# Kernel optimization log

Measured on AMD Instinct MI355X. Metric: run time of the kernel, lower is better.

The kernel has to match this reference:

```python
import jax, jax.numpy as jnp
import numpy as np

SIGMA_LOW = 0.2
SIGMA_HIGH = 0.01
DT = 0.1


def _gauss_kernel(sigma):
    # tw always uses sigma_low for its range, as in the original __init__
    tw = jnp.arange(-3.0 * SIGMA_LOW, 3.0 * SIGMA_LOW, 0.001 * DT, dtype=jnp.float32)  # 12000 taps
    g = jnp.exp(-0.5 * (tw / sigma) ** 2)
    return g / jnp.sum(g)


def _same_corr_fft(x, w):
    """tf.nn.conv1d(x, w_shared, stride=1, padding='SAME') where the same 1-D
    kernel w is applied to every channel independently (shared-weight depthwise).
    x: (1, T, C) NWC, w: (K,). FFT-based since K=12000 taps."""
    T = x.shape[1]
    K = w.shape[0]
    N = T + K - 1                      # full linear correlation length
    pad_left = (K - 1) // 2            # TF SAME left padding
    Xf = jnp.fft.rfft(x, n=N, axis=1)
    Wf = jnp.fft.rfft(w[::-1], n=N)    # flip kernel: correlation via convolution
    z = jnp.fft.irfft(Xf * Wf[None, :, None], n=N, axis=1)  # (1, N, C)
    start = K - 1 - pad_left           # offset of SAME output inside full result
    return jax.lax.dynamic_slice_in_dim(z, start, T, axis=1)


def setup_inputs() -> dict:
    key = jax.random.key(0)
    firings = jax.random.normal(key, (1, 100000, 512), dtype=jnp.float32)
    sel_idx = jnp.arange(256, dtype=jnp.int32)  # static boolean mask -> gather indices
    return {
        "firings": firings,
        "gauss_low": _gauss_kernel(SIGMA_LOW),
        "gauss_high": _gauss_kernel(SIGMA_HIGH),
        "sel_idx": sel_idx,
    }


def reference(firings, gauss_low, gauss_high, sel_idx):
    # boolean_mask(firings, mask, axis=2) -> channel gather
    sel = jnp.take(firings, sel_idx, axis=2)              # (1, T, Csel)
    low = _same_corr_fft(sel, gauss_low)                  # low-pass component
    filt = sel - low + jnp.mean(low)                      # high-pass + restore global mean
    return _same_corr_fft(filt, gauss_high)               # smooth with narrow Gaussian
```

## Files before the change

### kernel.cpp

```cpp
#include <hip/hip_runtime.h>
#include <hip/hip_bf16.h>

#define T_LEN   100000
#define C_SEL   256
#define C_IN    512
#define KLOW    12000
#define B1      50
#define NB1     2000
#define ND1     2001
#define NW1     241
#define ND2E    5003
#define WH_OFF  5500
#define KH      1001
#define MLEN    5000
#define TR      50
#define NBLK    2000
#define NAC     53
#define NSLOT   21
#define PROW    ((size_t)ND2E*C_SEL)

typedef __attribute__((ext_vector_type(4))) float f32x4;

__device__ __forceinline__ float rf(float x){
  return __int_as_float(__builtin_amdgcn_readfirstlane(__float_as_int(x)));
}

__device__ __forceinline__ void stage16(const float* g, float* l){
  __builtin_amdgcn_global_load_lds((const __attribute__((address_space(1))) void*)g,
                                   (__attribute__((address_space(3))) void*)l,
                                   16, 0, 0);
}

__global__ __launch_bounds__(256) void kA_prep(const float* __restrict__ wlow,
                                               const float* __restrict__ whigh,
                                               float* __restrict__ W1,
                                               float* __restrict__ musum,
                                               float* __restrict__ cwh,
                                               float* __restrict__ wht){
  if (blockIdx.x == 0){
    int m1 = threadIdx.x;
    if (m1 == 0) musum[0] = 0.f;
    if (m1 < NW1){
      float s = 0.f;
      int kbase = 50*m1 - 1;
      for (int off = 0; off < 50; ++off){
        int k = kbase + off;
        if (k >= 0 && k < KLOW) s += wlow[k];
      }
      W1[m1] = s * (1.0f/50.0f);
    }
    for (int k = threadIdx.x; k < 20*51; k += 256){
      int pp = k / 51, u = k - 51*pp;
      int j = 20*u + pp - 1;
      wht[k] = (j >= 0 && j < KH) ? whigh[WH_OFF + j] : 0.f;
    }
  } else {
    __shared__ float part[256];
    __shared__ float pre[257];
    int tg = threadIdx.x;
    float s = 0.f;
    #pragma unroll
    for (int r = 0; r < 4; ++r){ int j = 4*tg + r; if (j < KH) s += whigh[WH_OFF + j]; }
    part[tg] = s;
    __syncthreads();
    if (tg == 0){
      float run = 0.f; pre[0] = 0.f;
      for (int k = 0; k < 256; ++k){ run += part[k]; pre[k+1] = run; }
      cwh[0] = 0.f;
    }
    __syncthreads();
    float base = pre[tg], r0 = 0.f;
    #pragma unroll
    for (int r = 0; r < 4; ++r){
      int j = 4*tg + r;
      if (j < KH){ r0 += whigh[WH_OFF + j]; cwh[j+1] = base + r0; }
    }
  }
}

template<int PAR>
__device__ __forceinline__ void tile_conv(const float (*tile)[C_SEL],
                                          const float* __restrict__ wht,
                                          int tid, float* acc, float& ssum){
  #pragma unroll 1
  for (int pp = 0; pp < 10; ++pp){
    float tp[51];
    #pragma unroll
    for (int u = 0; u < 51; ++u) tp[u] = rf(wht[pp*51 + u]);
    if (PAR == 0){
      float v0 = tile[pp][tid], v1 = tile[20+pp][tid], v2 = tile[40+pp][tid];
      ssum += v0 + v1 + v2;
      #pragma unroll
      for (int u = 0; u < 51; ++u){
        acc[50-u] += tp[u]*v0; acc[51-u] += tp[u]*v1; acc[52-u] += tp[u]*v2;
      }
    } else {
      float v1 = tile[10+pp][tid], v2 = tile[30+pp][tid];
      ssum += v1 + v2;
      #pragma unroll
      for (int u = 0; u < 51; ++u){
        acc[51-u] += tp[u]*v1; acc[52-u] += tp[u]*v2;
      }
    }
  }
  #pragma unroll 1
  for (int pp = 10; pp < 20; ++pp){
    float tp[51];
    #pragma unroll
    for (int u = 0; u < 51; ++u) tp[u] = rf(wht[pp*51 + u]);
    if (PAR == 0){
      float v0 = tile[pp][tid], v1 = tile[20+pp][tid];
      ssum += v0 + v1;
      #pragma unroll
      for (int u = 0; u < 51; ++u){
        acc[50-u] += tp[u]*v0; acc[51-u] += tp[u]*v1;
      }
    } else {
      float v0 = tile[pp-10][tid], v1 = tile[pp+10][tid], v2 = tile[pp+30][tid];
      ssum += v0 + v1 + v2;
      #pragma unroll
      for (int u = 0; u < 51; ++u){
        acc[50-u] += tp[u]*v0; acc[51-u] += tp[u]*v1; acc[52-u] += tp[u]*v2;
      }
    }
  }
}

template<int PAR>
__device__ __forceinline__ void tile_store(const float* acc, int mbase, int b,
                                           int tid, float* __restrict__ pbuf){
  float* pb = pbuf + (size_t)(b % NSLOT)*PROW + tid;
  #pragma unroll
  for (int a = (PAR ? 1 : 0); a < NAC; ++a){
    int jo = mbase - 24 + a;
    if (jo >= 0 && jo < ND2E) pb[(size_t)jo*C_SEL] = acc[a];
  }
}

__global__ __launch_bounds__(256) void kC_conv(const float* __restrict__ x,
                                               const int* __restrict__ sel,
                                               const float* __restrict__ wht,
                                               float* __restrict__ S,
                                               float* __restrict__ pbuf){
  __shared__ float tile[TR][C_SEL];
  __shared__ int okf;
  int tid = threadIdx.x;
  int b   = blockIdx.x;
  int lane = tid & 63, wid = tid >> 6;
  if (tid == 0) okf = 1;
  __syncthreads();
  if (sel[tid] != tid) okf = 0;
  __syncthreads();
  const float* xrow0 = x + (size_t)b*(TR*C_IN);
  if (okf){
    for (int i = wid; i < TR; i += 4)
      stage16(xrow0 + (size_t)i*C_IN + 4*lane, &tile[i][0]);
    asm volatile("s_waitcnt vmcnt(0)" ::: "memory");
    __syncthreads();
  } else {
    int sc = sel[tid];
    for (int i = 0; i < TR; ++i) tile[i][tid] = xrow0[(size_t)i*C_IN + sc];
    __syncthreads();
  }
  float acc[NAC];
  #pragma unroll
  for (int a = 0; a < NAC; ++a) acc[a] = 0.f;
  float ssum = 0.f;
  int mbase = (b >> 1)*5 + (b & 1)*2;
  if (b & 1){ tile_conv<1>(tile, wht, tid, acc, ssum); tile_store<1>(acc, mbase, b, tid, pbuf); }
  else      { tile_conv<0>(tile, wht, tid, acc, ssum); tile_store<0>(acc, mbase, b, tid, pbuf); }
  S[b*C_SEL + tid] = ssum;
}

__global__ __launch_bounds__(256) void kB_lowd(const float* __restrict__ S,
                                               const float* __restrict__ W1,
                                               float* __restrict__ lowd,
                                               float* __restrict__ musum){
  __shared__ float w1s[NW1];
  int tid = threadIdx.x;
  if (tid < NW1) w1s[tid] = W1[tid];
  __syncthreads();
  int jd   = blockIdx.x*4 + (tid >> 6);
  int lane = tid & 63;
  if (jd >= ND1) return;
  int lo = 120 - jd;  if (lo < 0)   lo = 0;
  int hi = 2119 - jd; if (hi > 240) hi = 240;
  f32x4 acc = {0.f, 0.f, 0.f, 0.f};
  for (int m1 = lo; m1 <= hi; ++m1){
    int jb = jd + m1 - 120;
    acc += w1s[m1] * *reinterpret_cast<const f32x4*>(S + (size_t)jb*C_SEL + 4*lane);
  }
  *reinterpret_cast<f32x4*>(lowd + (size_t)jd*C_SEL + 4*lane) = acc;
  float t = acc.x + acc.y + acc.z + acc.w;
  for (int off = 32; off > 0; off >>= 1) t += __shfl_down(t, off);
  if (lane == 0){
    float ew = (jd == 0) ? 25.5f : ((jd == ND1-1) ? 24.5f : 50.f);
    atomicAdd(musum, ew*t);
  }
}

__global__ __launch_bounds__(256) void kC_red(const float* __restrict__ pbuf,
                                              const float* __restrict__ cwh,
                                              const float* __restrict__ lowd,
                                              const float* __restrict__ musum,
                                              float* __restrict__ outd){
  int tid = threadIdx.x;
  int jo  = blockIdx.x*4 + (tid >> 6);
  int j   = tid & 63;
  if (jo >= ND2E) return;
  int tlo = 20*jo - 519; if (tlo < 0) tlo = 0;
  int thi = 20*jo + 481; if (thi > T_LEN-1) thi = T_LEN-1;
  int blo = tlo/TR, bhi = thi/TR;
  f32x4 a = {0.f, 0.f, 0.f, 0.f};
  for (int b = blo; b <= bhi; ++b)
    a += *reinterpret_cast<const f32x4*>(pbuf + (size_t)(b % NSLOT)*PROW + (size_t)jo*C_SEL + 4*j);
  float mu = musum[0] * (1.0f/((float)T_LEN*(float)C_SEL));
  int tn = 20*(jo - 1);
  int jmin = 499 - tn;             if (jmin < 0) jmin = 0;
  int jmax = T_LEN - 1 + 499 - tn; if (jmax > 1000) jmax = 1000;
  float s = cwh[jmax + 1] - cwh[jmin];
  int tc = tn < 0 ? 0 : (tn > T_LEN-1 ? T_LEN-1 : tn);
  int jd = tc/50, rr = tc - 50*jd;
  float fr = rr*(1.f/50.f);
  f32x4 l0 = *reinterpret_cast<const f32x4*>(lowd + (size_t)jd*C_SEL + 4*j);
  f32x4 l1 = *reinterpret_cast<const f32x4*>(lowd + (size_t)(jd+1)*C_SEL + 4*j);
  f32x4 lo = l0 + (l1 - l0)*fr;
  *reinterpret_cast<f32x4*>(outd + (size_t)jo*C_SEL + 4*j) = a + (mu - lo)*s;
}

__global__ __launch_bounds__(256) void kD_interp(const float* __restrict__ outd,
                                                 float* __restrict__ out){
  int tid  = threadIdx.x;
  int lane = tid & 63;
  int w    = tid >> 6;
  int t0   = blockIdx.x*8;
  #pragma unroll
  for (int k = 0; k < 2; ++k){
    int t = t0 + w + 4*k;
    int jo = t/20, rr = t - jo*20;
    float a = rr*(1.f/20.f);
    const float* bb = outd + (size_t)jo*C_SEL + 4*lane;
    f32x4 p0 = *reinterpret_cast<const f32x4*>(bb);
    f32x4 p1 = *reinterpret_cast<const f32x4*>(bb +   C_SEL);
    f32x4 p2 = *reinterpret_cast<const f32x4*>(bb + 2*C_SEL);
    f32x4 p3 = *reinterpret_cast<const f32x4*>(bb + 3*C_SEL);
    f32x4 m = p1 + 0.5f*a*((p2 - p0)
            + a*((2.f*p0 - 5.f*p1 + 4.f*p2 - p3)
            + a*(3.f*(p1 - p2) + p3 - p0)));
    *reinterpret_cast<f32x4*>(out + (size_t)t*C_SEL + 4*lane) = m;
  }
}

extern "C" void kernel_launch(void* const* d_in, const int* in_sizes, int n_in,
                              void* d_out, int out_size, void* d_ws, size_t ws_size,
                              hipStream_t stream){
  const float* firings = (const float*)d_in[0];
  const float* glow    = (const float*)d_in[1];
  const float* ghigh   = (const float*)d_in[2];
  const int*   sel     = (const int*)d_in[3];
  float* out = (float*)d_out;
  float* ws  = (float*)d_ws;

  float* W1    = ws;
  float* musum = ws + 256;
  float* cwh   = ws + 320;
  float* wht   = ws + 1344;
  float* S     = ws + 2560;
  float* lowd  = ws + 514560;
  float* outd  = ws + 1026816;
  float* pbuf  = ws + 2307584;

  hipLaunchKernelGGL(kA_prep,  dim3(2),        dim3(256), 0, stream,
                     glow, ghigh, W1, musum, cwh, wht);
  hipLaunchKernelGGL(kC_conv,  dim3(NBLK),     dim3(256), 0, stream,
                     firings, sel, wht, S, pbuf);
  hipLaunchKernelGGL(kB_lowd,  dim3(501),      dim3(256), 0, stream, S, W1, lowd, musum);
  hipLaunchKernelGGL(kC_red,   dim3(1251),     dim3(256), 0, stream,
                     pbuf, cwh, lowd, musum, outd);
  hipLaunchKernelGGL(kD_interp,dim3(T_LEN/8),  dim3(256), 0, stream, outd, out);
}
```

Measured before the change: 426.3 us.

## Interleave partial-sum slots per output row and stage filter taps in LDS

The partial-sum buffer layout changes from slot-major to row-major with slots interleaved, so the reduction kernel reads all 21 slots of an output row contiguously and masks out the invalid ones instead of looping over a variable block range. The high-pass filter taps are staged once into LDS with padding to 52 per phase and loaded as float4 vectors, replacing per-tap global loads that went through readfirstlane. The low-pass accumulation loop is also unrolled by four. Reading every slot unconditionally costs extra bandwidth when fewer slots are valid, and the LDS tap reads are issued per lane instead of once as scalar values.

```diff
diff --git a/kernel.cpp b/kernel.cpp
--- a/kernel.cpp
+++ b/kernel.cpp
@@ -17,13 +17,8 @@
 #define NBLK    2000
 #define NAC     53
 #define NSLOT   21
-#define PROW    ((size_t)ND2E*C_SEL)
 
 typedef __attribute__((ext_vector_type(4))) float f32x4;
-
-__device__ __forceinline__ float rf(float x){
-  return __int_as_float(__builtin_amdgcn_readfirstlane(__float_as_int(x)));
-}
 
 __device__ __forceinline__ void stage16(const float* g, float* l){
   __builtin_amdgcn_global_load_lds((const __attribute__((address_space(1))) void*)g,
@@ -80,47 +75,53 @@
 
 template<int PAR>
 __device__ __forceinline__ void tile_conv(const float (*tile)[C_SEL],
-                                          const float* __restrict__ wht,
+                                          const float* __restrict__ whtl,
                                           int tid, float* acc, float& ssum){
   #pragma unroll 1
   for (int pp = 0; pp < 10; ++pp){
-    float tp[51];
-    #pragma unroll
-    for (int u = 0; u < 51; ++u) tp[u] = rf(wht[pp*51 + u]);
+    f32x4 tpc[13];
+    #pragma unroll
+    for (int c = 0; c < 13; ++c)
+      tpc[c] = *reinterpret_cast<const f32x4*>(&whtl[pp*52 + 4*c]);
     if (PAR == 0){
       float v0 = tile[pp][tid], v1 = tile[20+pp][tid], v2 = tile[40+pp][tid];
       ssum += v0 + v1 + v2;
       #pragma unroll
       for (int u = 0; u < 51; ++u){
-        acc[50-u] += tp[u]*v0; acc[51-u] += tp[u]*v1; acc[52-u] += tp[u]*v2;
+        float tp = tpc[u>>2][u&3];
+        acc[50-u] += tp*v0; acc[51-u] += tp*v1; acc[52-u] += tp*v2;
       }
     } else {
       float v1 = tile[10+pp][tid], v2 = tile[30+pp][tid];
       ssum += v1 + v2;
       #pragma unroll
       for (int u = 0; u < 51; ++u){
-        acc[51-u] += tp[u]*v1; acc[52-u] += tp[u]*v2;
+        float tp = tpc[u>>2][u&3];
+        acc[51-u] += tp*v1; acc[52-u] += tp*v2;
       }
     }
   }
   #pragma unroll 1
   for (int pp = 10; pp < 20; ++pp){
-    float tp[51];
-    #pragma unroll
-    for (int u = 0; u < 51; ++u) tp[u] = rf(wht[pp*51 + u]);
+    f32x4 tpc[13];
+    #pragma unroll
+    for (int c = 0; c < 13; ++c)
+      tpc[c] = *reinterpret_cast<const f32x4*>(&whtl[pp*52 + 4*c]);
     if (PAR == 0){
       float v0 = tile[pp][tid], v1 = tile[20+pp][tid];
       ssum += v0 + v1;
       #pragma unroll
       for (int u = 0; u < 51; ++u){
-        acc[50-u] += tp[u]*v0; acc[51-u] += tp[u]*v1;
+        float tp = tpc[u>>2][u&3];
+        acc[50-u] += tp*v0; acc[51-u] += tp*v1;
       }
     } else {
       float v0 = tile[pp-10][tid], v1 = tile[pp+10][tid], v2 = tile[pp+30][tid];
       ssum += v0 + v1 + v2;
       #pragma unroll
       for (int u = 0; u < 51; ++u){
-        acc[50-u] += tp[u]*v0; acc[51-u] += tp[u]*v1; acc[52-u] += tp[u]*v2;
+        float tp = tpc[u>>2][u&3];
+        acc[50-u] += tp*v0; acc[51-u] += tp*v1; acc[52-u] += tp*v2;
       }
     }
   }
@@ -129,11 +130,11 @@
 template<int PAR>
 __device__ __forceinline__ void tile_store(const float* acc, int mbase, int b,
                                            int tid, float* __restrict__ pbuf){
-  float* pb = pbuf + (size_t)(b % NSLOT)*PROW + tid;
+  float* pb = pbuf + (size_t)(b % NSLOT)*C_SEL + tid;
   #pragma unroll
   for (int a = (PAR ? 1 : 0); a < NAC; ++a){
     int jo = mbase - 24 + a;
-    if (jo >= 0 && jo < ND2E) pb[(size_t)jo*C_SEL] = acc[a];
+    if (jo >= 0 && jo < ND2E) pb[(size_t)jo*(NSLOT*C_SEL)] = acc[a];
   }
 }
 
@@ -143,6 +144,7 @@
                                                float* __restrict__ S,
                                                float* __restrict__ pbuf){
   __shared__ float tile[TR][C_SEL];
+  __shared__ float whtl[20*52];
   __shared__ int okf;
   int tid = threadIdx.x;
   int b   = blockIdx.x;
@@ -150,6 +152,10 @@
   if (tid == 0) okf = 1;
   __syncthreads();
   if (sel[tid] != tid) okf = 0;
+  for (int k = tid; k < 20*52; k += 256){
+    int pp = k / 52, u = k - 52*pp;
+    whtl[k] = (u < 51) ? wht[pp*51 + u] : 0.f;
+  }
   __syncthreads();
   const float* xrow0 = x + (size_t)b*(TR*C_IN);
   if (okf){
@@ -167,8 +173,8 @@
   for (int a = 0; a < NAC; ++a) acc[a] = 0.f;
   float ssum = 0.f;
   int mbase = (b >> 1)*5 + (b & 1)*2;
-  if (b & 1){ tile_conv<1>(tile, wht, tid, acc, ssum); tile_store<1>(acc, mbase, b, tid, pbuf); }
-  else      { tile_conv<0>(tile, wht, tid, acc, ssum); tile_store<0>(acc, mbase, b, tid, pbuf); }
+  if (b & 1){ tile_conv<1>(tile, whtl, tid, acc, ssum); tile_store<1>(acc, mbase, b, tid, pbuf); }
+  else      { tile_conv<0>(tile, whtl, tid, acc, ssum); tile_store<0>(acc, mbase, b, tid, pbuf); }
   S[b*C_SEL + tid] = ssum;
 }
 
@@ -186,6 +192,7 @@
   int lo = 120 - jd;  if (lo < 0)   lo = 0;
   int hi = 2119 - jd; if (hi > 240) hi = 240;
   f32x4 acc = {0.f, 0.f, 0.f, 0.f};
+  #pragma unroll 4
   for (int m1 = lo; m1 <= hi; ++m1){
     int jb = jd + m1 - 120;
     acc += w1s[m1] * *reinterpret_cast<const f32x4*>(S + (size_t)jb*C_SEL + 4*lane);
@@ -211,9 +218,20 @@
   int tlo = 20*jo - 519; if (tlo < 0) tlo = 0;
   int thi = 20*jo + 481; if (thi > T_LEN-1) thi = T_LEN-1;
   int blo = tlo/TR, bhi = thi/TR;
+  int cnt = bhi - blo + 1;
+  int sb  = blo % NSLOT;
+  const float* base = pbuf + (size_t)jo*(NSLOT*C_SEL) + 4*j;
   f32x4 a = {0.f, 0.f, 0.f, 0.f};
-  for (int b = blo; b <= bhi; ++b)
-    a += *reinterpret_cast<const f32x4*>(pbuf + (size_t)(b % NSLOT)*PROW + (size_t)jo*C_SEL + 4*j);
+  #pragma unroll
+  for (int k = 0; k < NSLOT; ++k){
+    f32x4 v = *reinterpret_cast<const f32x4*>(base + (size_t)k*C_SEL);
+    int d = k - sb; if (d < 0) d += NSLOT;
+    bool ok = (d < cnt);
+    a.x += ok ? v.x : 0.f;
+    a.y += ok ? v.y : 0.f;
+    a.z += ok ? v.z : 0.f;
+    a.w += ok ? v.w : 0.f;
+  }
   float mu = musum[0] * (1.0f/((float)T_LEN*(float)C_SEL));
   int tn = 20*(jo - 1);
   int jmin = 499 - tn;             if (jmin < 0) jmin = 0;
```

New measurement: 396.7 us. 7.0% less time.
